# Kernel tuning notes

Measured on AMD Instinct MI355X. Metric: run time of the kernel, lower is better.

The kernel has to match this reference:

```python
import jax, jax.numpy as jnp
import numpy as np

N = 50000          # num nodes
IN_DIM = 256       # input feature dim
OUT_DIM = 64       # output dim
SUPPORT = 8        # num relations
NUM_BASES = 4
NNZ = 800000       # nonzeros in sparse A [N, SUPPORT*N]


def setup_inputs() -> dict:
    key = jax.random.key(0)
    ks = jax.random.split(key, 6)
    E = jax.random.normal(ks[0], (N, IN_DIM), dtype=jnp.float32)
    W_F = jax.random.normal(ks[1], (NUM_BASES, IN_DIM, OUT_DIM), dtype=jnp.float32) * 0.05
    W_F_comp = jax.random.normal(ks[2], (SUPPORT, NUM_BASES), dtype=jnp.float32)
    b = jnp.zeros((OUT_DIM,), dtype=jnp.float32)
    A_vals = jax.random.uniform(ks[3], (NNZ,), dtype=jnp.float32)
    A_rows = jax.random.randint(ks[4], (NNZ,), 0, N, dtype=jnp.int32)
    A_cols = jax.random.randint(ks[5], (NNZ,), 0, SUPPORT * N, dtype=jnp.int32)
    return {"E": E, "W_F": W_F, "W_F_comp": W_F_comp, "b": b,
            "A_vals": A_vals, "A_rows": A_rows, "A_cols": A_cols}


def reference(E, W_F, W_F_comp, b, A_vals, A_rows, A_cols):
    # Basis decomposition: per-relation weights W[s] = sum_b comp[s,b] * W_F[b]
    # (matches transpose/einsum/transpose chain in the original call())
    W = jnp.einsum('sb,bio->sio', W_F_comp, W_F)          # [S, in, out]
    # Dense feature transform per relation, then flatten relation blocks
    FW = jnp.einsum('ni,sio->sno', E, W)                  # [S, N, out]
    FW = FW.reshape(SUPPORT * N, OUT_DIM)                 # [S*N, out]
    # Sparse A [N, S*N] @ FW  (tf.sparse_tensor_dense_matmul)
    msgs = A_vals[:, None] * FW[A_cols]                   # [nnz, out] gather
    AXW = jax.ops.segment_sum(msgs, A_rows, num_segments=N)  # [N, out] scatter-add
    return jax.nn.relu(AXW + b)
```

## Files before the change

### kernel.cpp

```cpp
#include <hip/hip_runtime.h>
#include <hip/hip_bf16.h>

typedef unsigned int  uint32;
typedef __attribute__((ext_vector_type(8))) short short8;
typedef __attribute__((ext_vector_type(4))) float f32x4;

#define NNODES   50000
#define IN_DIM   256
#define OUT_DIM  64
#define SUPPORT  8
#define NUM_BASES 4
#define NNZ      800000

#define M_PAD    50048
#define NBIG     512
#define CAP      64

#define EBF_OFF  0u
#define BK_OFF   0u
#define WT_OFF   25624576u
#define FW_OFF   25886720u
#define CNT_OFF  77086720u

__device__ __forceinline__ unsigned short f2bf_rne(float f) {
    uint32 u = __float_as_uint(f);
    u = (u + 0x7fffu + ((u >> 16) & 1u)) >> 16;
    return (unsigned short)u;
}
__device__ __forceinline__ float bf2f(unsigned short b) {
    return __uint_as_float(((uint32)b) << 16);
}
__device__ __forceinline__ void load_lds16(const void* g, void* l) {
    __builtin_amdgcn_global_load_lds(
        (const __attribute__((address_space(1))) void*)g,
        (__attribute__((address_space(3))) void*)l, 16, 0, 0);
}

__global__ __launch_bounds__(256) void cast_e_kernel(
    const float* __restrict__ E, unsigned short* __restrict__ Ebf)
{
    const int i8 = blockIdx.x * 256 + threadIdx.x;
    if (i8 >= M_PAD * IN_DIM / 8) return;
    unsigned short o[8];
    if (i8 < NNODES * IN_DIM / 8) {
        const float4 f0 = reinterpret_cast<const float4*>(E)[i8 * 2];
        const float4 f1 = reinterpret_cast<const float4*>(E)[i8 * 2 + 1];
        o[0]=f2bf_rne(f0.x); o[1]=f2bf_rne(f0.y); o[2]=f2bf_rne(f0.z); o[3]=f2bf_rne(f0.w);
        o[4]=f2bf_rne(f1.x); o[5]=f2bf_rne(f1.y); o[6]=f2bf_rne(f1.z); o[7]=f2bf_rne(f1.w);
    } else {
        #pragma unroll
        for (int j = 0; j < 8; ++j) o[j] = 0;
    }
    reinterpret_cast<ulonglong2*>(Ebf)[i8] = *reinterpret_cast<ulonglong2*>(o);
}

__global__ __launch_bounds__(256) void build_wbigt_kernel(
    const float* __restrict__ WF, const float* __restrict__ comp,
    unsigned short* __restrict__ WT)
{
    const int n = blockIdx.x;
    const int k = threadIdx.x;
    const int o = n & 63, s = n >> 6;
    float v = 0.f;
    #pragma unroll
    for (int b = 0; b < NUM_BASES; ++b)
        v = fmaf(comp[s * 4 + b], WF[(b * IN_DIM + k) * OUT_DIM + o], v);
    WT[n * IN_DIM + k] = f2bf_rne(v);
}

__global__ __launch_bounds__(256) void gemm_mfma_kernel(
    const unsigned short* __restrict__ Ebf,
    const unsigned short* __restrict__ WT,
    unsigned short* __restrict__ FW)
{
    __shared__ short Alds[128 * 64];
    __shared__ short Blds[128 * 64];

    const int tid  = threadIdx.x;
    const int lane = tid & 63;
    const int wid  = tid >> 6;
    const int wr   = wid >> 1;
    const int wc   = wid & 1;
    const int m0   = blockIdx.x * 128;
    const int n0   = blockIdx.y * 128;

    f32x4 acc[4][4];
    #pragma unroll
    for (int i = 0; i < 4; ++i)
        #pragma unroll
        for (int j = 0; j < 4; ++j) acc[i][j] = (f32x4){0.f, 0.f, 0.f, 0.f};

    const int srow = lane >> 3;
    const int scol = (lane & 7) * 16;

    for (int kt = 0; kt < 4; ++kt) {
        #pragma unroll
        for (int i = 0; i < 4; ++i) {
            const int c   = wid * 4 + i;
            const int row = c * 8 + srow;
            load_lds16(
                (const char*)Ebf + (size_t)(m0 + row) * 512 + kt * 128 + scol,
                (char*)Alds + c * 1024);
            load_lds16(
                (const char*)WT + (size_t)(n0 + row) * 512 + kt * 128 + scol,
                (char*)Blds + c * 1024);
        }
        __syncthreads();

        #pragma unroll
        for (int ks = 0; ks < 2; ++ks) {
            short8 af[4], bf[4];
            const int k0 = ks * 32 + (lane >> 4) * 8;
            #pragma unroll
            for (int mi = 0; mi < 4; ++mi)
                af[mi] = *reinterpret_cast<const short8*>(
                    &Alds[(wr * 64 + mi * 16 + (lane & 15)) * 64 + k0]);
            #pragma unroll
            for (int ni = 0; ni < 4; ++ni)
                bf[ni] = *reinterpret_cast<const short8*>(
                    &Blds[(wc * 64 + ni * 16 + (lane & 15)) * 64 + k0]);
            #pragma unroll
            for (int mi = 0; mi < 4; ++mi)
                #pragma unroll
                for (int ni = 0; ni < 4; ++ni)
                    acc[mi][ni] = __builtin_amdgcn_mfma_f32_16x16x32_bf16(
                        af[mi], bf[ni], acc[mi][ni], 0, 0, 0);
        }
        __syncthreads();
    }

    #pragma unroll
    for (int mi = 0; mi < 4; ++mi) {
        #pragma unroll
        for (int r = 0; r < 4; ++r) {
            const int row = m0 + wr * 64 + mi * 16 + (lane >> 4) * 4 + r;
            if (row < NNODES) {
                #pragma unroll
                for (int ni = 0; ni < 4; ++ni) {
                    const int col = n0 + wc * 64 + ni * 16 + (lane & 15);
                    FW[((size_t)(col >> 6) * NNODES + row) * 64 + (col & 63)]
                        = f2bf_rne(acc[mi][ni][r]);
                }
            }
        }
    }
}

__global__ __launch_bounds__(256) void fill_kernel(
    const float* __restrict__ vals, const int* __restrict__ rows,
    const int* __restrict__ cols, int* __restrict__ cnt,
    int2* __restrict__ bucket)
{
    const int e = blockIdx.x * 256 + threadIdx.x;
    if (e >= NNZ) return;
    const int r = rows[e];
    const int p = atomicAdd(&cnt[r], 1);
    if (p < CAP)
        bucket[r * CAP + p] = make_int2(cols[e], __float_as_int(vals[e]));
}

__global__ __launch_bounds__(256) void scatter_csr_kernel(
    const int* __restrict__ cnt, const int2* __restrict__ bucket,
    const unsigned short* __restrict__ FW, const float* __restrict__ bias,
    float* __restrict__ out)
{
    const int lane = threadIdx.x & 63;
    const int r    = blockIdx.x * 4 + (threadIdx.x >> 6);
    if (r >= NNODES) return;

    const int n = min(cnt[r], CAP);
    const int2 my = bucket[r * CAP + lane];

    float a0 = 0.f, a1 = 0.f, a2 = 0.f, a3 = 0.f;
    int j = 0;
    for (; j + 4 <= n; j += 4) {
        const uint32 c0 = (uint32)__builtin_amdgcn_readlane(my.x, j);
        const uint32 c1 = (uint32)__builtin_amdgcn_readlane(my.x, j + 1);
        const uint32 c2 = (uint32)__builtin_amdgcn_readlane(my.x, j + 2);
        const uint32 c3 = (uint32)__builtin_amdgcn_readlane(my.x, j + 3);
        const float  v0 = __int_as_float(__builtin_amdgcn_readlane(my.y, j));
        const float  v1 = __int_as_float(__builtin_amdgcn_readlane(my.y, j + 1));
        const float  v2 = __int_as_float(__builtin_amdgcn_readlane(my.y, j + 2));
        const float  v3 = __int_as_float(__builtin_amdgcn_readlane(my.y, j + 3));
        const unsigned short f0 = FW[(size_t)c0 * 64 + lane];
        const unsigned short f1 = FW[(size_t)c1 * 64 + lane];
        const unsigned short f2 = FW[(size_t)c2 * 64 + lane];
        const unsigned short f3 = FW[(size_t)c3 * 64 + lane];
        a0 = fmaf(v0, bf2f(f0), a0);
        a1 = fmaf(v1, bf2f(f1), a1);
        a2 = fmaf(v2, bf2f(f2), a2);
        a3 = fmaf(v3, bf2f(f3), a3);
    }
    for (; j < n; ++j) {
        const uint32 c = (uint32)__builtin_amdgcn_readlane(my.x, j);
        const float  v = __int_as_float(__builtin_amdgcn_readlane(my.y, j));
        a0 = fmaf(v, bf2f(FW[(size_t)c * 64 + lane]), a0);
    }
    const float acc = (a0 + a1) + (a2 + a3);
    out[(size_t)r * OUT_DIM + lane] = fmaxf(acc + bias[lane], 0.f);
}

extern "C" void kernel_launch(void* const* d_in, const int* in_sizes, int n_in,
                              void* d_out, int out_size, void* d_ws, size_t ws_size,
                              hipStream_t stream) {
    const float* E     = (const float*)d_in[0];
    const float* WF    = (const float*)d_in[1];
    const float* comp  = (const float*)d_in[2];
    const float* b     = (const float*)d_in[3];
    const float* Avals = (const float*)d_in[4];
    const int*   Arows = (const int*)d_in[5];
    const int*   Acols = (const int*)d_in[6];
    float* out = (float*)d_out;

    char* ws = (char*)d_ws;
    unsigned short* Ebf = (unsigned short*)(ws + EBF_OFF);
    unsigned short* WT  = (unsigned short*)(ws + WT_OFF);
    unsigned short* FW  = (unsigned short*)(ws + FW_OFF);
    int*   cnt    = (int*)(ws + CNT_OFF);
    int2*  bucket = (int2*)(ws + BK_OFF);

    cast_e_kernel<<<M_PAD * IN_DIM / 8 / 256, 256, 0, stream>>>(E, Ebf);
    build_wbigt_kernel<<<NBIG, 256, 0, stream>>>(WF, comp, WT);
    gemm_mfma_kernel<<<dim3(M_PAD / 128, NBIG / 128), 256, 0, stream>>>(Ebf, WT, FW);

    hipMemsetAsync(cnt, 0, NNODES * sizeof(int), stream);
    fill_kernel<<<(NNZ + 255) / 256, 256, 0, stream>>>(
        Avals, Arows, Acols, cnt, bucket);

    scatter_csr_kernel<<<(NNODES + 3) / 4, 256, 0, stream>>>(
        cnt, bucket, FW, b, out);
}
```

Baseline: 209.4 us.

## Fuse cast with weight build, and co-schedule GEMM with CSR bucket fill

Merges the E cast and basis-weight construction into one launch. It also merges the MFMA GEMM and the atomic bucket-fill into a single kernel, interleaving one fill block per three GEMM blocks so the memory-bound fill overlaps the compute-bound GEMM. The bucket moves to its own workspace region because it used to alias Ebf, and the per-row bucket capacity is lowered to 48, with the scatter guarding lanes beyond it. This cuts launch count and idle tail time, but rows with more than 48 entries would be truncated.

```diff
diff --git a/kernel.cpp b/kernel.cpp
--- a/kernel.cpp
+++ b/kernel.cpp
@@ -14,13 +14,19 @@
 
 #define M_PAD    50048
 #define NBIG     512
-#define CAP      64
+#define CAP      48
+
+#define GEMM_BLOCKS 1564
+#define FILL_BLOCKS 512
+#define MEGA_BLOCKS 2076
+#define CAST_BLOCKS 6256
+#define CW_BLOCKS   (CAST_BLOCKS + NBIG)
 
 #define EBF_OFF  0u
-#define BK_OFF   0u
 #define WT_OFF   25624576u
 #define FW_OFF   25886720u
 #define CNT_OFF  77086720u
+#define BK_OFF   77286720u
 
 __device__ __forceinline__ unsigned short f2bf_rne(float f) {
     uint32 u = __float_as_uint(f);
@@ -36,11 +42,27 @@
         (__attribute__((address_space(3))) void*)l, 16, 0, 0);
 }
 
-__global__ __launch_bounds__(256) void cast_e_kernel(
-    const float* __restrict__ E, unsigned short* __restrict__ Ebf)
+__global__ __launch_bounds__(256) void cast_wbig_kernel(
+    const float* __restrict__ E, unsigned short* __restrict__ Ebf,
+    const float* __restrict__ WF, const float* __restrict__ comp,
+    unsigned short* __restrict__ WT)
 {
-    const int i8 = blockIdx.x * 256 + threadIdx.x;
-    if (i8 >= M_PAD * IN_DIM / 8) return;
+    const int bid = blockIdx.x;
+    const int tid = threadIdx.x;
+
+    if (bid >= CAST_BLOCKS) {
+        const int n = bid - CAST_BLOCKS;
+        const int k = tid;
+        const int o = n & 63, s = n >> 6;
+        float v = 0.f;
+        #pragma unroll
+        for (int b = 0; b < NUM_BASES; ++b)
+            v = fmaf(comp[s * 4 + b], WF[(b * IN_DIM + k) * OUT_DIM + o], v);
+        WT[n * IN_DIM + k] = f2bf_rne(v);
+        return;
+    }
+
+    const int i8 = bid * 256 + tid;
     unsigned short o[8];
     if (i8 < NNODES * IN_DIM / 8) {
         const float4 f0 = reinterpret_cast<const float4*>(E)[i8 * 2];
@@ -54,35 +76,43 @@
     reinterpret_cast<ulonglong2*>(Ebf)[i8] = *reinterpret_cast<ulonglong2*>(o);
 }
 
-__global__ __launch_bounds__(256) void build_wbigt_kernel(
-    const float* __restrict__ WF, const float* __restrict__ comp,
-    unsigned short* __restrict__ WT)
-{
-    const int n = blockIdx.x;
-    const int k = threadIdx.x;
-    const int o = n & 63, s = n >> 6;
-    float v = 0.f;
-    #pragma unroll
-    for (int b = 0; b < NUM_BASES; ++b)
-        v = fmaf(comp[s * 4 + b], WF[(b * IN_DIM + k) * OUT_DIM + o], v);
-    WT[n * IN_DIM + k] = f2bf_rne(v);
-}
-
-__global__ __launch_bounds__(256) void gemm_mfma_kernel(
+__global__ __launch_bounds__(256) void mega_kernel(
     const unsigned short* __restrict__ Ebf,
     const unsigned short* __restrict__ WT,
-    unsigned short* __restrict__ FW)
+    unsigned short* __restrict__ FW,
+    const float* __restrict__ vals, const int* __restrict__ rows,
+    const int* __restrict__ cols, int* __restrict__ cnt,
+    int2* __restrict__ bucket)
 {
     __shared__ short Alds[128 * 64];
     __shared__ short Blds[128 * 64];
 
-    const int tid  = threadIdx.x;
+    const int bid = blockIdx.x;
+    const int tid = threadIdx.x;
+
+    int g;
+    if (bid < 2048) {
+        if ((bid & 3) == 3) {
+            for (int e = (bid >> 2) * 256 + tid; e < NNZ; e += FILL_BLOCKS * 256) {
+                const int r = rows[e];
+                const int p = atomicAdd(&cnt[r], 1);
+                if (p < CAP)
+                    bucket[(size_t)r * CAP + p] =
+                        make_int2(cols[e], __float_as_int(vals[e]));
+            }
+            return;
+        }
+        g = 3 * (bid >> 2) + (bid & 3);
+    } else {
+        g = 1536 + (bid - 2048);
+    }
+
     const int lane = tid & 63;
     const int wid  = tid >> 6;
     const int wr   = wid >> 1;
     const int wc   = wid & 1;
-    const int m0   = blockIdx.x * 128;
-    const int n0   = blockIdx.y * 128;
+    const int m0   = (g % 391) * 128;
+    const int n0   = (g / 391) * 128;
 
     f32x4 acc[4][4];
     #pragma unroll
@@ -146,19 +176,6 @@
     }
 }
 
-__global__ __launch_bounds__(256) void fill_kernel(
-    const float* __restrict__ vals, const int* __restrict__ rows,
-    const int* __restrict__ cols, int* __restrict__ cnt,
-    int2* __restrict__ bucket)
-{
-    const int e = blockIdx.x * 256 + threadIdx.x;
-    if (e >= NNZ) return;
-    const int r = rows[e];
-    const int p = atomicAdd(&cnt[r], 1);
-    if (p < CAP)
-        bucket[r * CAP + p] = make_int2(cols[e], __float_as_int(vals[e]));
-}
-
 __global__ __launch_bounds__(256) void scatter_csr_kernel(
     const int* __restrict__ cnt, const int2* __restrict__ bucket,
     const unsigned short* __restrict__ FW, const float* __restrict__ bias,
@@ -169,7 +186,8 @@
     if (r >= NNODES) return;
 
     const int n = min(cnt[r], CAP);
-    const int2 my = bucket[r * CAP + lane];
+    int2 my = make_int2(0, 0);
+    if (lane < CAP) my = bucket[(size_t)r * CAP + lane];
 
     float a0 = 0.f, a1 = 0.f, a2 = 0.f, a3 = 0.f;
     int j = 0;
@@ -219,13 +237,12 @@
     int*   cnt    = (int*)(ws + CNT_OFF);
     int2*  bucket = (int2*)(ws + BK_OFF);
 
-    cast_e_kernel<<<M_PAD * IN_DIM / 8 / 256, 256, 0, stream>>>(E, Ebf);
-    build_wbigt_kernel<<<NBIG, 256, 0, stream>>>(WF, comp, WT);
-    gemm_mfma_kernel<<<dim3(M_PAD / 128, NBIG / 128), 256, 0, stream>>>(Ebf, WT, FW);
-
     hipMemsetAsync(cnt, 0, NNODES * sizeof(int), stream);
-    fill_kernel<<<(NNZ + 255) / 256, 256, 0, stream>>>(
-        Avals, Arows, Acols, cnt, bucket);
+
+    cast_wbig_kernel<<<CW_BLOCKS, 256, 0, stream>>>(E, Ebf, WF, comp, WT);
+
+    mega_kernel<<<MEGA_BLOCKS, 256, 0, stream>>>(
+        Ebf, WT, FW, Avals, Arows, Acols, cnt, bucket);
 
     scatter_csr_kernel<<<(NNODES + 3) / 4, 256, 0, stream>>>(
         cnt, bucket, FW, b, out);
```

Measured after the change: 220.4 us. 1.05x slower.
